# Kernel tuning notes

Hardware: AMD Instinct MI355X
Metric: run time of the kernel (lower is better)

Reference implementation:

```python
import jax, jax.numpy as jnp
from jax import lax
import numpy as np

HEADS, SAMPLES = 4, 8
B, C, D, H, W = 1, 64, 16, 64, 64
HD = C // HEADS  # head_dim = 16
BN_EPS = 1e-5


def conv3d(x, w, b=None, pad=0):
    out = lax.conv_general_dilated(
        x, w, (1, 1, 1), [(pad, pad)] * 3,
        dimension_numbers=("NCDHW", "OIDHW", "NCDHW"))
    if b is not None:
        out = out + b[None, :, None, None, None]
    return out


def trilinear_sample(vol, grid):
    # vol: [Dv,Hv,Wv,Cc]; grid: [...,3] with torch grid_sample semantics:
    # grid[...,0] -> x (W axis), grid[...,1] -> y (H axis), grid[...,2] -> z (D axis)
    # align_corners=True, padding_mode='border'. Returns [..., Cc].
    Dv, Hv, Wv, _ = vol.shape
    ix = (grid[..., 0] + 1.0) * 0.5 * (Wv - 1)
    iy = (grid[..., 1] + 1.0) * 0.5 * (Hv - 1)
    iz = (grid[..., 2] + 1.0) * 0.5 * (Dv - 1)
    x0 = jnp.floor(ix); y0 = jnp.floor(iy); z0 = jnp.floor(iz)
    wx = (ix - x0)[..., None]; wy = (iy - y0)[..., None]; wz = (iz - z0)[..., None]
    x0i = jnp.clip(x0.astype(jnp.int32), 0, Wv - 1); x1i = jnp.clip(x0i + 1, 0, Wv - 1)
    y0i = jnp.clip(y0.astype(jnp.int32), 0, Hv - 1); y1i = jnp.clip(y0i + 1, 0, Hv - 1)
    z0i = jnp.clip(z0.astype(jnp.int32), 0, Dv - 1); z1i = jnp.clip(z0i + 1, 0, Dv - 1)
    g = lambda z, y, x: vol[z, y, x]
    out = (g(z0i, y0i, x0i) * (1 - wz) * (1 - wy) * (1 - wx)
           + g(z0i, y0i, x1i) * (1 - wz) * (1 - wy) * wx
           + g(z0i, y1i, x0i) * (1 - wz) * wy * (1 - wx)
           + g(z0i, y1i, x1i) * (1 - wz) * wy * wx
           + g(z1i, y0i, x0i) * wz * (1 - wy) * (1 - wx)
           + g(z1i, y0i, x1i) * wz * (1 - wy) * wx
           + g(z1i, y1i, x0i) * wz * wy * (1 - wx)
           + g(z1i, y1i, x1i) * wz * wy * wx)
    return out


def t_deform(feat_prev, feat_curr, p):
    b, c, d, h, w = feat_curr.shape
    kv = conv3d(feat_prev, p["kv_w"], p["kv_b"])          # [B,2C,D,H,W]
    q = conv3d(feat_curr, p["q_w"], p["q_b"])              # [B,C,D,H,W]
    # offset branch: conv3x3 -> GELU(exact) -> conv3x3(no bias) -> tanh
    o = conv3d(feat_curr, p["off1_w"], p["off1_b"], pad=1)
    o = jax.nn.gelu(o, approximate=False)
    o = jnp.tanh(conv3d(o, p["off2_w"], None, pad=1))      # [B,M*S*3,D,H,W]
    off = o.reshape(b, HEADS, SAMPLES, 3, d, h, w).transpose(0, 1, 4, 5, 6, 2, 3)  # [B,M,D,H,W,S,3]
    zz, yy, xx = jnp.meshgrid(jnp.linspace(-1, 1, d), jnp.linspace(-1, 1, h),
                              jnp.linspace(-1, 1, w), indexing="ij")
    base = jnp.stack((zz, yy, xx), axis=-1).astype(feat_curr.dtype)  # [D,H,W,3]
    scale = jnp.array([d, h, w], dtype=feat_curr.dtype)
    grid = base[None, None, :, :, :, None, :] + off / scale
    grid = jnp.clip(grid, -1.0, 1.0)
    grid = grid.transpose(0, 1, 5, 2, 3, 4, 6).reshape(b * HEADS, SAMPLES, d, h, w, 3)
    # channels-last per (batch,head) volume; avoids torch's explicit repeat over samples
    vols = kv.reshape(b, HEADS, 2 * HD, d, h, w).transpose(0, 1, 3, 4, 5, 2)
    vols = vols.reshape(b * HEADS, d, h, w, 2 * HD)
    sampled = jax.vmap(trilinear_sample)(vols, grid)        # [B*M,S,D,H,W,2*HD]
    sampled = sampled.reshape(b, HEADS, SAMPLES, d, h, w, 2 * HD)
    key, value = sampled[..., :HD], sampled[..., HD:]
    qh = q.reshape(b, HEADS, HD, d, h, w) * (HD ** -0.5)
    attn = jnp.einsum("bmcdhw,bmsdhwc->bmsdhw", qh, key)
    attn = jax.nn.softmax(attn, axis=2)
    fused = jnp.einsum("bmsdhw,bmsdhwc->bmcdhw", attn, value).reshape(b, c, d, h, w)
    out = conv3d(fused, p["out_w"], p["out_b"])
    # BatchNorm3d (eval: running stats) + ReLU
    inv = lax.rsqrt(p["bn_var"] + BN_EPS)
    out = (out - p["bn_mean"][None, :, None, None, None]) * (inv * p["bn_gamma"])[None, :, None, None, None] \
          + p["bn_beta"][None, :, None, None, None]
    return jax.nn.relu(out)


def setup_inputs() -> dict:
    key = jax.random.key(0)
    ks = jax.random.split(key, 16)
    r = lambda k, shp, s=0.05: (jax.random.normal(k, shp, dtype=jnp.float32) * s)
    return {
        "mid_feat": jax.random.normal(ks[0], (B, C, D, H, W), dtype=jnp.float32),
        "occ_feat": jax.random.normal(ks[1], (B, C, D, H, W), dtype=jnp.float32),
        "prev_feat": jax.random.normal(ks[2], (B, C, D, H, W), dtype=jnp.float32),
        "off1_w": r(ks[3], (C, C, 3, 3, 3)), "off1_b": r(ks[4], (C,)),
        "off2_w": r(ks[5], (HEADS * SAMPLES * 3, C, 3, 3, 3)),
        "kv_w": r(ks[6], (2 * C, C, 1, 1, 1)), "kv_b": r(ks[7], (2 * C,)),
        "q_w": r(ks[8], (C, C, 1, 1, 1)), "q_b": r(ks[9], (C,)),
        "out_w": r(ks[10], (C, C, 1, 1, 1)), "out_b": r(ks[11], (C,)),
        "bn_gamma": jnp.ones((C,), jnp.float32), "bn_beta": jnp.zeros((C,), jnp.float32),
        "bn_mean": jnp.zeros((C,), jnp.float32), "bn_var": jnp.ones((C,), jnp.float32),
    }


def reference(mid_feat, occ_feat, prev_feat, off1_w, off1_b, off2_w, kv_w, kv_b,
              q_w, q_b, out_w, out_b, bn_gamma, bn_beta, bn_mean, bn_var):
    p = dict(off1_w=off1_w, off1_b=off1_b, off2_w=off2_w, kv_w=kv_w, kv_b=kv_b,
             q_w=q_w, q_b=q_b, out_w=out_w, out_b=out_b, bn_gamma=bn_gamma,
             bn_beta=bn_beta, bn_mean=bn_mean, bn_var=bn_var)
    d1 = t_deform(mid_feat, occ_feat, p)
    d2 = t_deform(mid_feat, prev_feat, p)
    return jnp.concatenate([mid_feat, d1, d2], axis=1)  # [B,3C,D,H,W]
```

## Files before the change

### kernel.cpp

```cpp
#include <hip/hip_runtime.h>
#include <math.h>

#define DD 16
#define HH 64
#define WW 64
#define VV (DD*HH*WW)
#define CC 64
#define NHEADS 4
#define NSAMP 8
#define HDIM 16

typedef unsigned int uint;
typedef unsigned short ushort;
typedef __attribute__((ext_vector_type(8))) short bf16x8;
typedef __attribute__((ext_vector_type(4))) float f32x4;

__device__ __forceinline__ float clampf(float v, float lo, float hi){ return fminf(fmaxf(v, lo), hi); }
__device__ __forceinline__ int imin(int a, int b){ return a < b ? a : b; }

__device__ __forceinline__ ushort f2bf(float f){
  uint u = __float_as_uint(f);
  uint r = (u + 0x7fffu + ((u>>16)&1u)) >> 16;
  return (ushort)r;
}
__device__ __forceinline__ uint packbf2(float a, float b){
  return (uint)f2bf(a) | ((uint)f2bf(b) << 16);
}
__device__ __forceinline__ float bflo(uint u){ return __uint_as_float(u << 16); }
__device__ __forceinline__ float bfhi(uint u){ return __uint_as_float(u & 0xffff0000u); }
__device__ __forceinline__ float bf2f(ushort u){ return __uint_as_float((uint)u << 16); }

__device__ __forceinline__ float fast_tanh(float x){
  float e = __expf(2.f*x);
  return 1.f - 2.f/(e + 1.f);
}

__device__ __forceinline__ bf16x8 make_af(const float* __restrict__ w, int mt, int ks, int lane){
  const float* p = w + (size_t)(mt*16 + (lane&15))*CC + ks*32 + ((lane>>4)<<3);
  float4 f0 = *reinterpret_cast<const float4*>(p);
  float4 f1 = *reinterpret_cast<const float4*>(p+4);
  union { uint4 u; bf16x8 b; } r;
  r.u.x = packbf2(f0.x, f0.y); r.u.y = packbf2(f0.z, f0.w);
  r.u.z = packbf2(f1.x, f1.y); r.u.w = packbf2(f1.z, f1.w);
  return r.b;
}

__device__ __forceinline__ void repack_wmfma_body(const float* __restrict__ w,
                                                  uint* __restrict__ o, int MG, int U){
  int j2 = U & 3;
  int m  = (U>>2) & 15;
  int q  = (U>>6) & 3;
  int rest = U >> 8;
  int g = rest % MG;
  int s = rest / MG;
  int tap = s >> 1, h = s & 1;
  int co = g*16 + m;
  int ci = h*32 + q*8 + j2*2;
  int base = co*1728 + ci*27 + tap;
  o[U] = packbf2(w[base], w[base + 27]);
}

template<int CO, int EPI>
__device__ void conv1_body(
    int bid, int tid,
    const float* __restrict__ xa, const float* __restrict__ xb,
    const float* __restrict__ wraw, const float* __restrict__ bias,
    void* __restrict__ outp, float* __restrict__ mcopy)
{
  constexpr int MT = CO/16;
  constexpr int MW = MT/4;
  __shared__ ushort xt[64*72];
  int lane = tid & 63;
  int g = __builtin_amdgcn_readfirstlane(tid >> 6);
  int q = lane >> 4, n = lane & 15;
  int call = bid >> 10;
  int v0 = (bid & 1023) * 64;
  bf16x8 afr[2][MW];
  #pragma unroll
  for (int ks=0; ks<2; ks++)
    #pragma unroll
    for (int mw=0; mw<MW; mw++)
      afr[ks][mw] = make_af(wraw, g*MW+mw, ks, lane);
  const float* x = call ? xb : xa;
  for (int it = tid; it < 64*32; it += 256){
    int vox = it & 63; int cp = it >> 6;
    float a = x[(size_t)(2*cp)*VV + v0 + vox];
    float b = x[(size_t)(2*cp+1)*VV + v0 + vox];
    if constexpr (EPI == 0){
      mcopy[(size_t)(2*cp)*VV + v0 + vox] = a;
      mcopy[(size_t)(2*cp+1)*VV + v0 + vox] = b;
    }
    *reinterpret_cast<uint*>(&xt[vox*72 + 2*cp]) = packbf2(a,b);
  }
  __syncthreads();
  f32x4 acc[MW][4];
  #pragma unroll
  for (int mw=0;mw<MW;mw++)
    #pragma unroll
    for (int nt=0;nt<4;nt++){ acc[mw][nt].x=0.f; acc[mw][nt].y=0.f; acc[mw][nt].z=0.f; acc[mw][nt].w=0.f; }
  const char* ldsb = reinterpret_cast<const char*>(xt);
  #pragma unroll
  for (int ks=0; ks<2; ks++){
    bf16x8 bfr[4];
    #pragma unroll
    for (int nt=0; nt<4; nt++)
      bfr[nt] = *reinterpret_cast<const bf16x8*>(ldsb + ((nt*16+n)*144 + q*16 + ks*64));
    #pragma unroll
    for (int mw=0; mw<MW; mw++)
      #pragma unroll
      for (int nt=0; nt<4; nt++)
        acc[mw][nt] = __builtin_amdgcn_mfma_f32_16x16x32_bf16(afr[ks][mw], bfr[nt], acc[mw][nt], 0, 0, 0);
  }
  if constexpr (EPI == 0){
    #pragma unroll
    for (int mw=0; mw<MW; mw++){
      int mt = g*MW + mw;
      int cob = mt*16 + q*4;
      #pragma unroll
      for (int nt=0; nt<4; nt++){
        int v = v0 + nt*16 + n;
        float r0 = acc[mw][nt].x + bias[cob+0];
        float r1 = acc[mw][nt].y + bias[cob+1];
        float r2 = acc[mw][nt].z + bias[cob+2];
        float r3 = acc[mw][nt].w + bias[cob+3];
        int z = v >> 12, y = (v >> 6) & 63, xx = v & 63;
        int head = cob >> 5;
        uint* vols = (uint*)outp;
        uint2 pk; pk.x = packbf2(r0,r1); pk.y = packbf2(r2,r3);
        *reinterpret_cast<uint2*>(vols + ((size_t)head*VV + (size_t)(y*WW+xx)*DD + z)*16 + ((cob&31)>>1)) = pk;
      }
    }
  } else {
    __syncthreads();
    ushort* xr = xt;
    int cob = g*16 + q*4;
    #pragma unroll
    for (int nt=0; nt<4; nt++){
      int vox = nt*16 + n;
      uint2 pk;
      pk.x = packbf2((acc[0][nt].x + bias[cob+0])*0.25f, (acc[0][nt].y + bias[cob+1])*0.25f);
      pk.y = packbf2((acc[0][nt].z + bias[cob+2])*0.25f, (acc[0][nt].w + bias[cob+3])*0.25f);
      *reinterpret_cast<uint2*>(&xr[vox*64 + cob]) = pk;
    }
    __syncthreads();
    char* ob = (char*)((ushort*)outp + (size_t)call*CC*VV) + (size_t)v0*128;
    const char* lb = reinterpret_cast<const char*>(xr);
    #pragma unroll
    for (int k=0; k<2; k++){
      int idx = tid + k*256;
      *reinterpret_cast<uint4*>(ob + idx*16) = *reinterpret_cast<const uint4*>(lb + idx*16);
    }
  }
}

__global__ __launch_bounds__(256) void fused_front(
    const float* __restrict__ occ, const float* __restrict__ prev,
    const float* __restrict__ mid, uint* __restrict__ o0pk,
    const float* __restrict__ off1w, uint* __restrict__ wA1,
    const float* __restrict__ off2w, uint* __restrict__ wA2,
    const float* __restrict__ kvw,  const float* __restrict__ kvb,
    const float* __restrict__ qw,   const float* __restrict__ qb,
    void* __restrict__ vols, void* __restrict__ qbuf, float* __restrict__ out)
{
  int b = blockIdx.x, tid = threadIdx.x;
  if (b < 2048){
    int idx = b*256 + tid;
    int v4 = (idx & (VV/4 - 1)) * 4;
    int rest = idx >> 14;
    int cq = rest & 15;
    int call = rest >> 4;
    const float* x = call ? prev : occ;
    const float* p0 = x + (size_t)(cq*4)*VV + v4;
    float4 f0 = *reinterpret_cast<const float4*>(p0);
    float4 f1 = *reinterpret_cast<const float4*>(p0 + VV);
    float4 f2 = *reinterpret_cast<const float4*>(p0 + 2*VV);
    float4 f3 = *reinterpret_cast<const float4*>(p0 + 3*VV);
    uint* ob = o0pk + ((size_t)(call*16 + cq)*VV + v4)*2;
    uint4 w0, w1;
    w0.x = packbf2(f0.x, f1.x); w0.y = packbf2(f2.x, f3.x);
    w0.z = packbf2(f0.y, f1.y); w0.w = packbf2(f2.y, f3.y);
    w1.x = packbf2(f0.z, f1.z); w1.y = packbf2(f2.z, f3.z);
    w1.z = packbf2(f0.w, f1.w); w1.w = packbf2(f2.w, f3.w);
    *reinterpret_cast<uint4*>(ob)     = w0;
    *reinterpret_cast<uint4*>(ob + 4) = w1;
  }
  else if (b < 2264){ repack_wmfma_body(off1w, wA1, 4, (b-2048)*256 + tid); }
  else if (b < 2588){ repack_wmfma_body(off2w, wA2, 6, (b-2264)*256 + tid); }
  else if (b < 3612){ conv1_body<128,0>(b-2588, tid, mid, nullptr, kvw, kvb, vols, out); }
  else              { conv1_body<64,1>(b-3612, tid, occ, prev, qw, qb, qbuf, nullptr); }
}

template<int CO, int OUTPK, int PREF>
__global__ __launch_bounds__(256) void conv3_mfma(
    const uint* __restrict__ xpk,
    const uint* __restrict__ wA, const float* __restrict__ bias,
    void* __restrict__ outp)
{
  constexpr int MG = CO/16;
  constexpr int MROW = CO/32;
  __shared__ ushort xh[24576];
  int tid = threadIdx.x;
  int lane = tid & 63;
  int w = __builtin_amdgcn_readfirstlane(tid >> 6);
  int q = lane >> 4, n = lane & 15;
  int bid = blockIdx.x;
  int xcd = bid & 7, islot = bid >> 3;
  int call = xcd >> 2;
  int z0 = (xcd & 3) * 4;
  int by = (islot >> 3) << 3, bx = (islot & 7) << 3;

  const uint2* xinp = reinterpret_cast<const uint2*>(xpk) + (size_t)call*16*VV;

  int mbase = (w & 1) * MROW;
  int nzh = (w >> 1) * 2;
  int lo[8];
  #pragma unroll
  for (int nt=0;nt<8;nt++){
    int zi = nzh + (nt>>2);
    int vl = (nt&3)*16 + n;
    lo[nt] = (zi*100 + (vl>>3)*10 + (vl&7))*80 + q*16;
  }
  f32x4 acc[MROW][8];
  #pragma unroll
  for (int mr=0;mr<MROW;mr++)
    #pragma unroll
    for (int nt=0;nt<8;nt++){ acc[mr][nt].x=0.f; acc[mr][nt].y=0.f; acc[mr][nt].z=0.f; acc[mr][nt].w=0.f; }

  const char* ldsb = reinterpret_cast<const char*>(xh);
  const char* wac  = reinterpret_cast<const char*>(wA);

  auto compute_half = [&](int h){
    #pragma unroll 2
    for (int tap=0; tap<27; tap++){
      int dz = tap/9; int r9 = tap - dz*9; int dy = r9/3; int dxx = r9 - dy*3;
      int stepOff = (dz*100 + dy*10 + dxx)*80;
      int s = tap*2 + h;
      bf16x8 af[MROW];
      #pragma unroll
      for (int mr=0;mr<MROW;mr++)
        af[mr] = *reinterpret_cast<const bf16x8*>(wac + (size_t)((s*MG + mbase+mr)*64 + lane)*16);
      bf16x8 bf[8];
      #pragma unroll
      for (int nt=0;nt<8;nt++)
        bf[nt] = *reinterpret_cast<const bf16x8*>(ldsb + (lo[nt] + stepOff));
      #pragma unroll
      for (int mr=0;mr<MROW;mr++)
        #pragma unroll
        for (int nt=0;nt<8;nt++)
          acc[mr][nt] = __builtin_amdgcn_mfma_f32_16x16x32_bf16(af[mr], bf[nt], acc[mr][nt], 0, 0, 0);
    }
  };

  if constexpr (PREF){
    uint2 pq[19];
    auto load_half = [&](int h){
      #pragma unroll
      for (int k=0;k<19;k++){
        int it = tid + k*256;
        if (it < 4800){
          int cg = it/600; int pos = it - cg*600;
          int dz = pos/100; int rr = pos - dz*100; int dy = rr/10; int dxx = rr - dy*10;
          int gz = z0 + dz - 1, gy = by + dy - 1, gx = bx + dxx - 1;
          uint2 v; v.x = 0u; v.y = 0u;
          if (gz>=0 && gz<DD && gy>=0 && gy<HH && gx>=0 && gx<WW)
            v = xinp[(size_t)(h*8+cg)*VV + (size_t)((gz*HH+gy)*WW + gx)];
          pq[k] = v;
        }
      }
    };
    auto write_half = [&](){
      #pragma unroll
      for (int k=0;k<19;k++){
        int it = tid + k*256;
        if (it < 4800){
          int cg = it/600; int pos = it - cg*600;
          *reinterpret_cast<uint2*>(&xh[pos*40 + cg*4]) = pq[k];
        }
      }
    };
    load_half(0);
    write_half();
    __syncthreads();
    load_half(1);
    compute_half(0);
    __syncthreads();
    write_half();
    __syncthreads();
    compute_half(1);
  } else {
    #pragma unroll 1
    for (int h=0; h<2; h++){
      if (h) __syncthreads();
      for (int k=0;k<19;k++){
        int it = tid + k*256;
        if (it < 4800){
          int cg = it/600; int pos = it - cg*600;
          int dz = pos/100; int rr = pos - dz*100; int dy = rr/10; int dxx = rr - dy*10;
          int gz = z0 + dz - 1, gy = by + dy - 1, gx = bx + dxx - 1;
          uint2 v; v.x = 0u; v.y = 0u;
          if (gz>=0 && gz<DD && gy>=0 && gy<HH && gx>=0 && gx<WW)
            v = xinp[(size_t)(h*8+cg)*VV + (size_t)((gz*HH+gy)*WW + gx)];
          *reinterpret_cast<uint2*>(&xh[pos*40 + cg*4]) = v;
        }
      }
      __syncthreads();
      compute_half(h);
    }
  }

  if (OUTPK == 1){
    #pragma unroll
    for (int mr=0; mr<MROW; mr++){
      int cob = (mbase+mr)*16 + q*4;
      #pragma unroll
      for (int nt=0; nt<8; nt++){
        int zi = nzh + (nt>>2);
        int vl = (nt&3)*16 + n;
        int vy = by + (vl>>3), vx = bx + (vl&7);
        size_t gv = (size_t)(((z0+zi)*HH + vy)*WW + vx);
        float r0 = acc[mr][nt].x + bias[cob+0];
        float r1 = acc[mr][nt].y + bias[cob+1];
        float r2 = acc[mr][nt].z + bias[cob+2];
        float r3 = acc[mr][nt].w + bias[cob+3];
        r0 = 0.5f*r0*(1.f + erff(r0*0.70710678118654752f));
        r1 = 0.5f*r1*(1.f + erff(r1*0.70710678118654752f));
        r2 = 0.5f*r2*(1.f + erff(r2*0.70710678118654752f));
        r3 = 0.5f*r3*(1.f + erff(r3*0.70710678118654752f));
        uint2 pk; pk.x = packbf2(r0,r1); pk.y = packbf2(r2,r3);
        uint* dst = (uint*)outp;
        *reinterpret_cast<uint2*>(dst + ((size_t)(call*16 + (cob>>2))*VV + gv)*2) = pk;
      }
    }
  } else {
    __syncthreads();
    ushort* xr = xh;
    #pragma unroll
    for (int mr=0; mr<MROW; mr++){
      int cob = (mbase+mr)*16 + q*4;
      #pragma unroll
      for (int nt=0; nt<8; nt++){
        int row = (nzh + (nt>>2))*64 + (nt&3)*16 + n;
        uint2 pk;
        pk.x = packbf2(fast_tanh(acc[mr][nt].x), fast_tanh(acc[mr][nt].y));
        pk.y = packbf2(fast_tanh(acc[mr][nt].z), fast_tanh(acc[mr][nt].w));
        *reinterpret_cast<uint2*>(&xr[row*96 + cob]) = pk;
      }
    }
    __syncthreads();
    ushort* dst = (ushort*)outp + (size_t)call*96*VV;
    const char* lb = reinterpret_cast<const char*>(xr);
    #pragma unroll
    for (int k=0; k<12; k++){
      int idx = tid + k*256;
      int chunk = idx/96;
      int off = idx - chunk*96;
      int zi = chunk>>3, y8 = chunk&7;
      size_t gb = (size_t)(((z0+zi)*HH + by + y8)*WW + bx)*192 + (size_t)off*16;
      *reinterpret_cast<uint4*>((char*)dst + gb) = *reinterpret_cast<const uint4*>(lb + idx*16);
    }
  }
}

struct Geom { int x0,x1,y0,y1,z0,z1; float wx,wy,wz; };
__device__ __forceinline__ Geom make_geom(float zb, float yb, float xb,
                                          float o0, float o1, float o2){
  float g0 = clampf(zb + o0*(1.f/16.f), -1.f, 1.f);
  float g1 = clampf(yb + o1*(1.f/64.f), -1.f, 1.f);
  float g2 = clampf(xb + o2*(1.f/64.f), -1.f, 1.f);
  float ix = (g0+1.f)*0.5f*63.f;
  float iy = (g1+1.f)*0.5f*63.f;
  float iz = (g2+1.f)*0.5f*15.f;
  float fx=floorf(ix), fy=floorf(iy), fz=floorf(iz);
  Geom g;
  g.wx = ix-fx; g.wy = iy-fy; g.wz = iz-fz;
  g.x0 = (int)fx; g.x1 = imin(g.x0+1, WW-1);
  g.y0 = (int)fy; g.y1 = imin(g.y0+1, HH-1);
  g.z0 = (int)fz; g.z1 = imin(g.z0+1, DD-1);
  return g;
}

__global__ __launch_bounds__(256) void sample_attn_kernel(
    const ushort* __restrict__ qbuf, const ushort* __restrict__ offbuf,
    const uint* __restrict__ vols, const float* __restrict__ outw,
    const float* __restrict__ outb, const float* __restrict__ bng,
    const float* __restrict__ bnb, const float* __restrict__ bnm,
    const float* __restrict__ bnv, float* __restrict__ dout)
{
  __shared__ ushort fsb[16*72];
  int t = threadIdx.x;
  int lane = t & 63;
  int m = __builtin_amdgcn_readfirstlane(t >> 6);
  int slot = lane >> 2;
  int r = lane & 3;
  int bid = blockIdx.x;
  int xcd = bid & 7, islot = bid >> 3;
  int call = islot >> 9;
  int z = xcd*2 + ((islot >> 8) & 1);
  int rem = islot & 255;
  int y = rem >> 2;
  int x0 = (rem & 3) << 4;
  int x = x0 + slot;
  int vbase = (z*HH + y)*WW + x0;
  int v = vbase + slot;

  const ushort* qb = qbuf   + (size_t)call*CC*VV;
  const ushort* ob = offbuf + (size_t)call*96*VV;

  uint4 qu = *reinterpret_cast<const uint4*>(qb + (size_t)v*64 + m*16 + (r&1)*8);
  float qf[8];
  qf[0]=bflo(qu.x); qf[1]=bfhi(qu.x); qf[2]=bflo(qu.y); qf[3]=bfhi(qu.y);
  qf[4]=bflo(qu.z); qf[5]=bfhi(qu.z); qf[6]=bflo(qu.w); qf[7]=bfhi(qu.w);

  uint ou[12];
  {
    const uint4* op4 = reinterpret_cast<const uint4*>(ob + (size_t)v*96 + m*24);
    uint4 a = op4[0], b4 = op4[1], c4 = op4[2];
    ou[0]=a.x;  ou[1]=a.y;  ou[2]=a.z;  ou[3]=a.w;
    ou[4]=b4.x; ou[5]=b4.y; ou[6]=b4.z; ou[7]=b4.w;
    ou[8]=c4.x; ou[9]=c4.y; ou[10]=c4.z; ou[11]=c4.w;
  }

  float zbf = -1.f + (float)z*(2.f/15.f);
  float ybf = -1.f + (float)y*(2.f/63.f);
  float xbf = -1.f + (float)x*(2.f/63.f);

  const char* volb = reinterpret_cast<const char*>(vols) + (size_t)m*VV*64;
  float roleK = (r < 2) ? 1.f : 0.f;
  float lrun = 0.f;
  float fused[8];
  #pragma unroll
  for (int c=0;c<8;c++) fused[c]=0.f;

  #pragma unroll
  for (int s=0;s<NSAMP;s++){
    int i0 = 3*s, i1 = 3*s+1, i2 = 3*s+2;
    float o0 = (i0&1) ? bfhi(ou[i0>>1]) : bflo(ou[i0>>1]);
    float o1 = (i1&1) ? bfhi(ou[i1>>1]) : bflo(ou[i1>>1]);
    float o2 = (i2&1) ? bfhi(ou[i2>>1]) : bflo(ou[i2>>1]);
    Geom g = make_geom(zbf,ybf,xbf,o0,o1,o2);
    int tz0 = g.z0*64 + r*16;
    int tz1 = g.z1*64 + r*16;
    float wx1 = g.wx, wx0 = 1.f-g.wx;
    float wy1 = g.wy, wy0 = 1.f-g.wy;
    float wz1 = g.wz, wz0 = 1.f-g.wz;
    float acc[8];
    #pragma unroll
    for (int c=0;c<8;c++) acc[c]=0.f;
    #pragma unroll
    for (int ky=0;ky<2;ky++)
    #pragma unroll
    for (int kx=0;kx<2;kx++){
      int cy = ky? g.y1:g.y0, cx = kx? g.x1:g.x0;
      float wyx = (ky? wy1:wy0)*(kx? wx1:wx0);
      float a0 = wyx*wz0, a1 = wyx*wz1;
      uint wzp;
      asm("v_cvt_pk_bf16_f32 %0, %1, %2" : "=v"(wzp) : "v"(a0), "v"(a1));
      int tb = ((cy<<6) + cx) << 10;
      const char* p = volb + tb;
      uint4 u0 = *reinterpret_cast<const uint4*>(p + tz0);
      uint4 u1 = *reinterpret_cast<const uint4*>(p + tz1);
      uint plo, phi;
      plo = __builtin_amdgcn_perm(u1.x, u0.x, 0x05040100u);
      phi = __builtin_amdgcn_perm(u1.x, u0.x, 0x07060302u);
      asm("v_dot2_f32_bf16 %0, %1, %2, %0" : "+v"(acc[0]) : "v"(plo), "v"(wzp));
      asm("v_dot2_f32_bf16 %0, %1, %2, %0" : "+v"(acc[1]) : "v"(phi), "v"(wzp));
      plo = __builtin_amdgcn_perm(u1.y, u0.y, 0x05040100u);
      phi = __builtin_amdgcn_perm(u1.y, u0.y, 0x07060302u);
      asm("v_dot2_f32_bf16 %0, %1, %2, %0" : "+v"(acc[2]) : "v"(plo), "v"(wzp));
      asm("v_dot2_f32_bf16 %0, %1, %2, %0" : "+v"(acc[3]) : "v"(phi), "v"(wzp));
      plo = __builtin_amdgcn_perm(u1.z, u0.z, 0x05040100u);
      phi = __builtin_amdgcn_perm(u1.z, u0.z, 0x07060302u);
      asm("v_dot2_f32_bf16 %0, %1, %2, %0" : "+v"(acc[4]) : "v"(plo), "v"(wzp));
      asm("v_dot2_f32_bf16 %0, %1, %2, %0" : "+v"(acc[5]) : "v"(phi), "v"(wzp));
      plo = __builtin_amdgcn_perm(u1.w, u0.w, 0x05040100u);
      phi = __builtin_amdgcn_perm(u1.w, u0.w, 0x07060302u);
      asm("v_dot2_f32_bf16 %0, %1, %2, %0" : "+v"(acc[6]) : "v"(plo), "v"(wzp));
      asm("v_dot2_f32_bf16 %0, %1, %2, %0" : "+v"(acc[7]) : "v"(phi), "v"(wzp));
    }
    float h = qf[0]*acc[0]+qf[1]*acc[1]+qf[2]*acc[2]+qf[3]*acc[3]
            + qf[4]*acc[4]+qf[5]*acc[5]+qf[6]*acc[6]+qf[7]*acc[7];
    h *= roleK;
    h += __shfl_xor(h, 1);
    h += __shfl_xor(h, 2);
    float e = __expf(h);
    lrun += e;
    #pragma unroll
    for (int c=0;c<8;c++) fused[c] += e*acc[c];
  }
  float isum = 1.f/lrun;
  if (r >= 2){
    uint4 pk;
    pk.x = packbf2(fused[0]*isum, fused[1]*isum);
    pk.y = packbf2(fused[2]*isum, fused[3]*isum);
    pk.z = packbf2(fused[4]*isum, fused[5]*isum);
    pk.w = packbf2(fused[6]*isum, fused[7]*isum);
    *reinterpret_cast<uint4*>(&fsb[slot*72 + m*16 + (r&1)*8]) = pk;
  }
  __syncthreads();

  int qq = lane >> 4, n = lane & 15;
  f32x4 acco;
  acco.x=0.f; acco.y=0.f; acco.z=0.f; acco.w=0.f;
  const char* ldsb = reinterpret_cast<const char*>(fsb);
  #pragma unroll
  for (int ks=0; ks<2; ks++){
    bf16x8 af = make_af(outw, m, ks, lane);
    bf16x8 bfv = *reinterpret_cast<const bf16x8*>(ldsb + (n*144 + qq*16 + ks*64));
    acco = __builtin_amdgcn_mfma_f32_16x16x32_bf16(af, bfv, acco, 0, 0, 0);
  }
  int choff = 64 + call*64;
  #pragma unroll
  for (int rr=0; rr<4; rr++){
    int co = m*16 + qq*4 + rr;
    float inv = rsqrtf(bnv[co] + 1e-5f) * bng[co];
    float val = (acco[rr] + outb[co] - bnm[co]) * inv + bnb[co];
    val = fmaxf(val, 0.f);
    dout[(size_t)(choff+co)*VV + vbase + n] = val;
  }
}

extern "C" void kernel_launch(void* const* d_in, const int* in_sizes, int n_in,
                              void* d_out, int out_size, void* d_ws, size_t ws_size,
                              hipStream_t stream){
  (void)in_sizes; (void)n_in; (void)out_size; (void)ws_size;
  const float* mid  = (const float*)d_in[0];
  const float* occ  = (const float*)d_in[1];
  const float* prev = (const float*)d_in[2];
  const float* off1w= (const float*)d_in[3];
  const float* off1b= (const float*)d_in[4];
  const float* off2w= (const float*)d_in[5];
  const float* kvw  = (const float*)d_in[6];
  const float* kvb  = (const float*)d_in[7];
  const float* qw   = (const float*)d_in[8];
  const float* qb   = (const float*)d_in[9];
  const float* outw = (const float*)d_in[10];
  const float* outb = (const float*)d_in[11];
  const float* bng  = (const float*)d_in[12];
  const float* bnb  = (const float*)d_in[13];
  const float* bnm  = (const float*)d_in[14];
  const float* bnv  = (const float*)d_in[15];
  float* out = (float*)d_out;

  uint*   vols  = (uint*)d_ws;
  ushort* qbuf  = (ushort*)(vols + (size_t)4*VV*16);
  uint*   o1pk  = (uint*)(qbuf + (size_t)2*CC*VV);
  ushort* offb  = (ushort*)(o1pk + (size_t)2*32*VV);
  uint*   wA1   = (uint*)(offb + (size_t)2*96*VV);
  uint*   wA2   = wA1 + 55296;
  uint*   o0pk  = wA2 + 82944;

  fused_front<<<5660, 256, 0, stream>>>(occ, prev, mid, o0pk,
      off1w, wA1, off2w, wA2, kvw, kvb, qw, qb,
      (void*)vols, (void*)qbuf, out);
  conv3_mfma<64,1,1><<<512, 256, 0, stream>>>(o0pk, wA1, off1b, (void*)o1pk);
  conv3_mfma<96,0,0><<<512, 256, 0, stream>>>(o1pk, wA2, off1b, (void*)offb);
  sample_attn_kernel<<<8192, 256, 0, stream>>>(qbuf, offb, vols, outw,
      outb, bng, bnb, bnm, bnv, out);
}
```

Baseline: 332.3 us.

## Widen packed bf16 channel groups to 8 and pre-repack output projection weights

Activations for the 3x3x3 conv are now packed as 8 bf16 channels per voxel (16-byte uint4) instead of 4, so the front pack, the conv3 LDS staging loads and the conv1 epilogue stores all move twice the data per access with half the instructions. The output projection weights are repacked once into MFMA fragment order in the front kernel, and sample_attn now loads them directly rather than converting fp32 weights in every block. This reduces global load instruction counts and per-block weight conversion, but changes the packed layout that several kernels must agree on.

```diff
diff --git a/kernel.cpp b/kernel.cpp
--- a/kernel.cpp
+++ b/kernel.cpp
@@ -58,6 +58,18 @@
   int ci = h*32 + q*8 + j2*2;
   int base = co*1728 + ci*27 + tap;
   o[U] = packbf2(w[base], w[base + 27]);
+}
+__device__ __forceinline__ void repack_w1_body(const float* __restrict__ w,
+                                               uint* __restrict__ o, int MT, int U){
+  int j2 = U & 3;
+  int lane = (U>>2) & 63;
+  int frag = U >> 8;
+  int mt = frag % MT;
+  int ks = frag / MT;
+  int q = lane >> 4, m = lane & 15;
+  int co = mt*16 + m;
+  int ci = ks*32 + q*8 + j2*2;
+  o[U] = packbf2(w[co*CC + ci], w[co*CC + ci + 1]);
 }
 
 template<int CO, int EPI>
@@ -158,36 +170,40 @@
     const float* __restrict__ mid, uint* __restrict__ o0pk,
     const float* __restrict__ off1w, uint* __restrict__ wA1,
     const float* __restrict__ off2w, uint* __restrict__ wA2,
+    const float* __restrict__ outw,  uint* __restrict__ wo,
     const float* __restrict__ kvw,  const float* __restrict__ kvb,
     const float* __restrict__ qw,   const float* __restrict__ qb,
     void* __restrict__ vols, void* __restrict__ qbuf, float* __restrict__ out)
 {
   int b = blockIdx.x, tid = threadIdx.x;
-  if (b < 2048){
+  if (b < 1024){
     int idx = b*256 + tid;
     int v4 = (idx & (VV/4 - 1)) * 4;
     int rest = idx >> 14;
-    int cq = rest & 15;
-    int call = rest >> 4;
+    int cg = rest & 7;
+    int call = rest >> 3;
     const float* x = call ? prev : occ;
-    const float* p0 = x + (size_t)(cq*4)*VV + v4;
-    float4 f0 = *reinterpret_cast<const float4*>(p0);
-    float4 f1 = *reinterpret_cast<const float4*>(p0 + VV);
-    float4 f2 = *reinterpret_cast<const float4*>(p0 + 2*VV);
-    float4 f3 = *reinterpret_cast<const float4*>(p0 + 3*VV);
-    uint* ob = o0pk + ((size_t)(call*16 + cq)*VV + v4)*2;
-    uint4 w0, w1;
-    w0.x = packbf2(f0.x, f1.x); w0.y = packbf2(f2.x, f3.x);
-    w0.z = packbf2(f0.y, f1.y); w0.w = packbf2(f2.y, f3.y);
-    w1.x = packbf2(f0.z, f1.z); w1.y = packbf2(f2.z, f3.z);
-    w1.z = packbf2(f0.w, f1.w); w1.w = packbf2(f2.w, f3.w);
-    *reinterpret_cast<uint4*>(ob)     = w0;
-    *reinterpret_cast<uint4*>(ob + 4) = w1;
-  }
-  else if (b < 2264){ repack_wmfma_body(off1w, wA1, 4, (b-2048)*256 + tid); }
-  else if (b < 2588){ repack_wmfma_body(off2w, wA2, 6, (b-2264)*256 + tid); }
-  else if (b < 3612){ conv1_body<128,0>(b-2588, tid, mid, nullptr, kvw, kvb, vols, out); }
-  else              { conv1_body<64,1>(b-3612, tid, occ, prev, qw, qb, qbuf, nullptr); }
+    const float* p0 = x + (size_t)(cg*8)*VV + v4;
+    float4 f[8];
+    #pragma unroll
+    for (int c=0;c<8;c++) f[c] = *reinterpret_cast<const float4*>(p0 + (size_t)c*VV);
+    uint4* ob = reinterpret_cast<uint4*>(o0pk) + (size_t)(call*8 + cg)*VV + v4;
+    #pragma unroll
+    for (int j=0;j<4;j++){
+      float* fp = reinterpret_cast<float*>(f);
+      uint4 w;
+      w.x = packbf2(fp[0*4+j], fp[1*4+j]);
+      w.y = packbf2(fp[2*4+j], fp[3*4+j]);
+      w.z = packbf2(fp[4*4+j], fp[5*4+j]);
+      w.w = packbf2(fp[6*4+j], fp[7*4+j]);
+      ob[j] = w;
+    }
+  }
+  else if (b < 1240){ repack_wmfma_body(off1w, wA1, 4, (b-1024)*256 + tid); }
+  else if (b < 1564){ repack_wmfma_body(off2w, wA2, 6, (b-1240)*256 + tid); }
+  else if (b < 1572){ repack_w1_body(outw, wo, 4, (b-1564)*256 + tid); }
+  else if (b < 2596){ conv1_body<128,0>(b-1572, tid, mid, nullptr, kvw, kvb, vols, out); }
+  else              { conv1_body<64,1>(b-2596, tid, occ, prev, qw, qb, qbuf, nullptr); }
 }
 
 template<int CO, int OUTPK, int PREF>
@@ -209,7 +225,7 @@
   int z0 = (xcd & 3) * 4;
   int by = (islot >> 3) << 3, bx = (islot & 7) << 3;
 
-  const uint2* xinp = reinterpret_cast<const uint2*>(xpk) + (size_t)call*16*VV;
+  const uint4* xinp = reinterpret_cast<const uint4*>(xpk) + (size_t)call*8*VV;
 
   int mbase = (w & 1) * MROW;
   int nzh = (w >> 1) * 2;
@@ -252,29 +268,29 @@
   };
 
   if constexpr (PREF){
-    uint2 pq[19];
+    uint4 pq[10];
     auto load_half = [&](int h){
       #pragma unroll
-      for (int k=0;k<19;k++){
+      for (int k=0;k<10;k++){
         int it = tid + k*256;
-        if (it < 4800){
+        if (it < 2400){
           int cg = it/600; int pos = it - cg*600;
           int dz = pos/100; int rr = pos - dz*100; int dy = rr/10; int dxx = rr - dy*10;
           int gz = z0 + dz - 1, gy = by + dy - 1, gx = bx + dxx - 1;
-          uint2 v; v.x = 0u; v.y = 0u;
+          uint4 v; v.x = 0u; v.y = 0u; v.z = 0u; v.w = 0u;
           if (gz>=0 && gz<DD && gy>=0 && gy<HH && gx>=0 && gx<WW)
-            v = xinp[(size_t)(h*8+cg)*VV + (size_t)((gz*HH+gy)*WW + gx)];
+            v = xinp[(size_t)(h*4+cg)*VV + (size_t)((gz*HH+gy)*WW + gx)];
           pq[k] = v;
         }
       }
     };
     auto write_half = [&](){
       #pragma unroll
-      for (int k=0;k<19;k++){
+      for (int k=0;k<10;k++){
         int it = tid + k*256;
-        if (it < 4800){
+        if (it < 2400){
           int cg = it/600; int pos = it - cg*600;
-          *reinterpret_cast<uint2*>(&xh[pos*40 + cg*4]) = pq[k];
+          *reinterpret_cast<uint4*>(&xh[pos*40 + cg*8]) = pq[k];
         }
       }
     };
@@ -291,16 +307,16 @@
     #pragma unroll 1
     for (int h=0; h<2; h++){
       if (h) __syncthreads();
-      for (int k=0;k<19;k++){
+      for (int k=0;k<10;k++){
         int it = tid + k*256;
-        if (it < 4800){
+        if (it < 2400){
           int cg = it/600; int pos = it - cg*600;
           int dz = pos/100; int rr = pos - dz*100; int dy = rr/10; int dxx = rr - dy*10;
           int gz = z0 + dz - 1, gy = by + dy - 1, gx = bx + dxx - 1;
-          uint2 v; v.x = 0u; v.y = 0u;
+          uint4 v; v.x = 0u; v.y = 0u; v.z = 0u; v.w = 0u;
           if (gz>=0 && gz<DD && gy>=0 && gy<HH && gx>=0 && gx<WW)
-            v = xinp[(size_t)(h*8+cg)*VV + (size_t)((gz*HH+gy)*WW + gx)];
-          *reinterpret_cast<uint2*>(&xh[pos*40 + cg*4]) = v;
+            v = xinp[(size_t)(h*4+cg)*VV + (size_t)((gz*HH+gy)*WW + gx)];
+          *reinterpret_cast<uint4*>(&xh[pos*40 + cg*8]) = v;
         }
       }
       __syncthreads();
@@ -328,7 +344,7 @@
         r3 = 0.5f*r3*(1.f + erff(r3*0.70710678118654752f));
         uint2 pk; pk.x = packbf2(r0,r1); pk.y = packbf2(r2,r3);
         uint* dst = (uint*)outp;
-        *reinterpret_cast<uint2*>(dst + ((size_t)(call*16 + (cob>>2))*VV + gv)*2) = pk;
+        *reinterpret_cast<uint2*>(dst + ((size_t)(call*8 + (cob>>3))*VV + gv)*4 + ((cob&4)>>1)) = pk;
       }
     }
   } else {
@@ -381,7 +397,7 @@
 
 __global__ __launch_bounds__(256) void sample_attn_kernel(
     const ushort* __restrict__ qbuf, const ushort* __restrict__ offbuf,
-    const uint* __restrict__ vols, const float* __restrict__ outw,
+    const uint* __restrict__ vols, const uint* __restrict__ woA,
     const float* __restrict__ outb, const float* __restrict__ bng,
     const float* __restrict__ bnb, const float* __restrict__ bnm,
     const float* __restrict__ bnv, float* __restrict__ dout)
@@ -502,9 +518,10 @@
   f32x4 acco;
   acco.x=0.f; acco.y=0.f; acco.z=0.f; acco.w=0.f;
   const char* ldsb = reinterpret_cast<const char*>(fsb);
+  const char* wac  = reinterpret_cast<const char*>(woA);
   #pragma unroll
   for (int ks=0; ks<2; ks++){
-    bf16x8 af = make_af(outw, m, ks, lane);
+    bf16x8 af = *reinterpret_cast<const bf16x8*>(wac + (size_t)((ks*4 + m)*64 + lane)*16);
     bf16x8 bfv = *reinterpret_cast<const bf16x8*>(ldsb + (n*144 + qq*16 + ks*64));
     acco = __builtin_amdgcn_mfma_f32_16x16x32_bf16(af, bfv, acco, 0, 0, 0);
   }
@@ -547,13 +564,14 @@
   ushort* offb  = (ushort*)(o1pk + (size_t)2*32*VV);
   uint*   wA1   = (uint*)(offb + (size_t)2*96*VV);
   uint*   wA2   = wA1 + 55296;
-  uint*   o0pk  = wA2 + 82944;
-
-  fused_front<<<5660, 256, 0, stream>>>(occ, prev, mid, o0pk,
-      off1w, wA1, off2w, wA2, kvw, kvb, qw, qb,
+  uint*   wo    = wA2 + 82944;
+  uint*   o0pk  = wo  + 2048;
+
+  fused_front<<<4644, 256, 0, stream>>>(occ, prev, mid, o0pk,
+      off1w, wA1, off2w, wA2, outw, wo, kvw, kvb, qw, qb,
       (void*)vols, (void*)qbuf, out);
   conv3_mfma<64,1,1><<<512, 256, 0, stream>>>(o0pk, wA1, off1b, (void*)o1pk);
   conv3_mfma<96,0,0><<<512, 256, 0, stream>>>(o1pk, wA2, off1b, (void*)offb);
-  sample_attn_kernel<<<8192, 256, 0, stream>>>(qbuf, offb, vols, outw,
+  sample_attn_kernel<<<8192, 256, 0, stream>>>(qbuf, offb, vols, wo,
       outb, bng, bnb, bnm, bnv, out);
 }
```

Measured after the change: 311.8 us. 6.2% less time.
